# Kernel tuning notes

Measured on AMD Instinct MI355X. Metric: run time of the kernel, lower is better.

The kernel has to match this reference:

```python
import jax, jax.numpy as jnp
import numpy as np

SCALE = 8
NUM_CLASSES = 15
IGNORE_THRES = 0.5
# anchors for scale=8 divided by scale
GRID_ANCHOR = jnp.array([[96.0 / 8, 230.0 / 8], [79.0 / 8, 186.0 / 8], [81.0 / 8, 133.0 / 8]], dtype=jnp.float32)  # [3,2]


def _bce_sum(p, t, mask):
    # torch BCELoss(reduction='sum') with log clamped at -100, restricted to mask
    lp = jnp.maximum(jnp.log(p), -100.0)
    ln = jnp.maximum(jnp.log(1.0 - p), -100.0)
    return jnp.sum(-(t * lp + (1.0 - t) * ln) * mask)


def setup_inputs() -> dict:
    key = jax.random.key(0)
    k1, k2, k3 = jax.random.split(key, 3)
    nB, nG = 128, 52
    x = jax.random.normal(k1, (nB, 3 * (NUM_CLASSES + 5), nG, nG), dtype=jnp.float32)
    boxes = jax.random.uniform(k2, (nB, 4), minval=0.1, maxval=0.6)  # cx,cy,w,h in (0,1)
    cls = jax.random.randint(k3, (nB, 1), 0, NUM_CLASSES).astype(jnp.float32)
    labels = jnp.concatenate([boxes, cls], axis=-1)  # [nB,5]
    return {"x": x, "labels": labels}


def reference(x, labels):
    nB, nG = x.shape[0], x.shape[2]
    pred = x.reshape(nB, 3, NUM_CLASSES + 5, nG, nG).transpose(0, 1, 3, 4, 2)  # [B,3,G,G,20]
    px = jax.nn.sigmoid(pred[..., 0])
    py = jax.nn.sigmoid(pred[..., 1])
    pw = pred[..., 2]
    ph = pred[..., 3]
    conf = jax.nn.sigmoid(pred[..., 4])
    cls = jax.nn.softmax(pred[..., 5:], axis=-1)
    pred_boxs = jnp.stack([px, py, pw, ph], axis=-1)  # [B,3,G,G,4]
    out = jnp.concatenate([
        pred_boxs.reshape(nB, -1, 4) * SCALE,
        conf.reshape(nB, -1, 1),
        cls.reshape(nB, -1, NUM_CLASSES),
    ], axis=-1)

    # ---- build_targets (vectorized; one target per image as in original loop) ----
    tb = labels[:, :4] * nG  # boxes in grid units [B,4]
    gx, gy, gw, gh = tb[:, 0], tb[:, 1], tb[:, 2], tb[:, 3]
    gi = gx.astype(jnp.int32)
    gj = gy.astype(jnp.int32)
    gcls = labels[:, 4].astype(jnp.int32)

    # wh-IoU anchors vs targets -> [3,B]
    aw, ah = GRID_ANCHOR[:, 0:1], GRID_ANCHOR[:, 1:2]
    inter_wh = jnp.minimum(aw, gw[None, :]) * jnp.minimum(ah, gh[None, :])
    ious = inter_wh / (aw * ah + 1e-16 + gw[None, :] * gh[None, :] - inter_wh)
    best_idx = jnp.argmax(ious, axis=0)  # [B]

    bidx = jnp.arange(nB)
    shape4 = (nB, 3, nG, nG)
    obj = jnp.zeros(shape4, jnp.float32).at[bidx, best_idx, gj, gi].set(1.0)

    noobj = jnp.ones(shape4, jnp.float32)
    arep = jnp.tile(jnp.arange(3), nB)
    brep = jnp.repeat(bidx, 3)
    jrep = jnp.repeat(gj, 3)
    irep = jnp.repeat(gi, 3)
    ign = (jnp.reshape(ious.T, (-1,)) > IGNORE_THRES).astype(jnp.float32)
    noobj = noobj.at[brep, arep, jrep, irep].mul(1.0 - ign)
    noobj = noobj.at[bidx, best_idx, gj, gi].set(0.0)

    gif = gi.astype(jnp.float32)
    gjf = gj.astype(jnp.float32)
    tx = jnp.zeros(shape4, jnp.float32).at[bidx, best_idx, gj, gi].set(gx - gif)
    ty = jnp.zeros(shape4, jnp.float32).at[bidx, best_idx, gj, gi].set(gy - gjf)
    tw = jnp.zeros(shape4, jnp.float32).at[bidx, best_idx, gj, gi].set(jnp.log(gw / GRID_ANCHOR[best_idx, 0] + 1e-16))
    th = jnp.zeros(shape4, jnp.float32).at[bidx, best_idx, gj, gi].set(jnp.log(gh / GRID_ANCHOR[best_idx, 1] + 1e-16))
    tcls = jnp.zeros(shape4 + (NUM_CLASSES,), jnp.float32).at[bidx, best_idx, gj, gi, gcls].set(1.0)

    # cls_mask: does argmax of predicted class at target cell match gt class
    pred_cls_at = cls[bidx, best_idx, gj, gi]  # [B,15]
    cls_hit = (jnp.argmax(pred_cls_at, axis=-1) == gcls).astype(jnp.float32)
    cls_mask = jnp.zeros(shape4, jnp.float32).at[bidx, best_idx, gj, gi].set(cls_hit)

    # iou between pred box at target cell and target box (cxcywh, +1 corner convention)
    pb = pred_boxs[bidx, best_idx, gj, gi]  # [B,4]
    b1x1, b1y1 = pb[:, 0] - pb[:, 2] / 2, pb[:, 1] - pb[:, 3] / 2
    b1x2, b1y2 = pb[:, 0] + pb[:, 2] / 2, pb[:, 1] + pb[:, 3] / 2
    b2x1, b2y1 = gx - gw / 2, gy - gh / 2
    b2x2, b2y2 = gx + gw / 2, gy + gh / 2
    iw = jnp.clip(jnp.minimum(b1x2, b2x2) - jnp.maximum(b1x1, b2x1) + 1, 0)
    ih = jnp.clip(jnp.minimum(b1y2, b2y2) - jnp.maximum(b1y1, b2y1) + 1, 0)
    inter = iw * ih
    a1 = (b1x2 - b1x1 + 1) * (b1y2 - b1y1 + 1)
    a2 = (b2x2 - b2x1 + 1) * (b2y2 - b2y1 + 1)
    iou_vec = inter / (a1 + a2 - inter + 1e-16)
    iou_scores = jnp.zeros(shape4, jnp.float32).at[bidx, best_idx, gj, gi].set(iou_vec)

    tconf = obj
    # ---- losses (boolean-mask indexing replaced by masked sums) ----
    loss_x = jnp.sum(jnp.abs(px - tx) * obj)
    loss_y = jnp.sum(jnp.abs(py - ty) * obj)
    loss_w = jnp.sum(jnp.abs(pw - tw) * obj)
    loss_h = jnp.sum(jnp.abs(ph - th) * obj)
    loss_conf = _bce_sum(conf, tconf, obj) + 100.0 * _bce_sum(conf, tconf, noobj)
    loss_cls = _bce_sum(cls, tcls, obj[..., None])
    loss = loss_x + loss_y + loss_w + loss_h + loss_conf + loss_cls
    return (loss, out)
```

## Files before the change

### kernel.cpp

```cpp
#include <hip/hip_runtime.h>
#include <math.h>

#define NB    128
#define NG    52
#define NGG   2704
#define NA    3
#define NCLS  15
#define NCH   20
#define NQ    8112
#define TOTAL 1038336
#define BLK   256
#define NBLK  (TOTAL/BLK)
#define WPB   (BLK/64)
#define FPW   (64*NCH)
#define NPART (NBLK*WPB)

typedef float f4 __attribute__((ext_vector_type(4)));

__global__ __launch_bounds__(BLK) void main_kernel(const float* __restrict__ x,
                                                   const float* __restrict__ labels,
                                                   float* __restrict__ out,
                                                   float* __restrict__ partials) {
    __shared__ __align__(16) float sm[WPB][FPW];

    int t = threadIdx.x;
    int w = t >> 6;
    int l = t & 63;
    int cell = blockIdx.x * BLK + t;
    int b  = cell / NQ;
    int r  = cell - b * NQ;
    int a  = r / NGG;
    int ji = r - a * NGG;

    const float* __restrict__ xp = x + ((size_t)(b*60 + a*20)) * NGG + ji;
    float z[NCH];
    #pragma unroll
    for (int c = 0; c < NCH; c++) z[c] = xp[c * NGG];

    float v[NCH];
    float conf = 1.0f / (1.0f + __expf(-z[4]));
    v[0] = 8.0f / (1.0f + __expf(-z[0]));
    v[1] = 8.0f / (1.0f + __expf(-z[1]));
    v[2] = 8.0f * z[2];
    v[3] = 8.0f * z[3];
    v[4] = conf;
    float m = z[5];
    #pragma unroll
    for (int c = 6; c < NCH; c++) m = fmaxf(m, z[c]);
    float s = 0.0f;
    #pragma unroll
    for (int c = 0; c < NCLS; c++) { v[5+c] = __expf(z[5+c] - m); s += v[5+c]; }
    float inv = 1.0f / s;
    #pragma unroll
    for (int c = 0; c < NCLS; c++) v[5+c] *= inv;

    float gx = labels[b*5+0] * (float)NG;
    float gy = labels[b*5+1] * (float)NG;
    float gw = labels[b*5+2] * (float)NG;
    float gh = labels[b*5+3] * (float)NG;
    int  gcls = (int)labels[b*5+4];
    int gi = (int)gx, gj = (int)gy;
    float gwgh = gw * gh;
    float i0 = fminf(12.0f,   gw) * fminf(28.75f,  gh);
    float i1 = fminf(9.875f,  gw) * fminf(23.25f,  gh);
    float i2 = fminf(10.125f, gw) * fminf(16.625f, gh);
    float iou0 = i0 / (345.0f      + 1e-16f + gwgh - i0);
    float iou1 = i1 / (229.59375f  + 1e-16f + gwgh - i1);
    float iou2 = i2 / (168.328125f + 1e-16f + gwgh - i2);
    int best = 0; float bv = iou0;
    if (iou1 > bv) { best = 1; bv = iou1; }
    if (iou2 > bv) { best = 2; bv = iou2; }
    float ioua = (a == 0) ? iou0 : ((a == 1) ? iou1 : iou2);
    bool at_t   = (ji == gj * NG + gi);
    bool isbest = (a == best);

    float tsum = 0.0f;
    if (!(at_t && (isbest || ioua > 0.5f)))
        tsum = -100.0f * fmaxf(__logf(1.0f - conf), -100.0f);
    if (at_t && isbest) {
        tsum += -fmaxf(__logf(conf), -100.0f);
        float txv = gx - (float)gi;
        float tyv = gy - (float)gj;
        float abw = (best == 0) ? 12.0f  : ((best == 1) ? 9.875f : 10.125f);
        float abh = (best == 0) ? 28.75f : ((best == 1) ? 23.25f : 16.625f);
        float twv = __logf(gw / abw + 1e-16f);
        float thv = __logf(gh / abh + 1e-16f);
        tsum += fabsf(v[0]*0.125f - txv) + fabsf(v[1]*0.125f - tyv)
              + fabsf(v[2]*0.125f - twv) + fabsf(v[3]*0.125f - thv);
        #pragma unroll
        for (int c = 0; c < NCLS; c++) {
            float p = v[5+c];
            tsum += (c == gcls) ? -fmaxf(__logf(p),        -100.0f)
                                : -fmaxf(__logf(1.0f - p), -100.0f);
        }
    }

    float* __restrict__ smw = sm[w];
    int base = l * NCH - 3;
    #pragma unroll
    for (int c = 0; c < NCH; c++) {
        int L = base + c;
        if (L < 0) L += FPW;
        smw[L] = v[c];
    }

    #pragma unroll
    for (int off = 32; off > 0; off >>= 1) tsum += __shfl_down(tsum, off, 64);

    int cell0 = blockIdx.x * BLK + w * 64;
    size_t gf = 1 + (size_t)cell0 * NCH;
    f4* __restrict__ op = (f4*)(out + gf + 3);
    const f4* __restrict__ sp = (const f4*)smw;
    #pragma unroll
    for (int k = 0; k < 5; k++) {
        int q = k * 64 + l;
        if (q < (FPW - 4) / 4) __builtin_nontemporal_store(sp[q], &op[q]);
    }
    if (l == 0) {
        out[gf + 0]       = smw[FPW - 3];
        out[gf + 1]       = smw[FPW - 2];
        out[gf + 2]       = smw[FPW - 1];
        out[gf + FPW - 1] = smw[FPW - 4];
        partials[blockIdx.x * WPB + w] = tsum;
    }
}

__global__ __launch_bounds__(1024) void finish_kernel(const float* __restrict__ partials,
                                                      float* __restrict__ out) {
    int t = threadIdx.x;
    float s = 0.0f;
    #pragma unroll
    for (int k = 0; k < NPART/1024 + 1; k++) {
        int q = k * 1024 + t;
        if (q < NPART) s += partials[q];
    }
    __shared__ float red[1024];
    red[t] = s;
    __syncthreads();
    for (int k = 512; k > 0; k >>= 1) {
        if (t < k) red[t] += red[t + k];
        __syncthreads();
    }
    if (t == 0) out[0] = red[0];
}

extern "C" void kernel_launch(void* const* d_in, const int* in_sizes, int n_in,
                              void* d_out, int out_size, void* d_ws, size_t ws_size,
                              hipStream_t stream) {
    const float* x      = (const float*)d_in[0];
    const float* labels = (const float*)d_in[1];
    float* out = (float*)d_out;
    float* ws  = (float*)d_ws;

    hipLaunchKernelGGL(main_kernel,   dim3(NBLK), dim3(BLK),  0, stream, x, labels, out, ws);
    hipLaunchKernelGGL(finish_kernel, dim3(1),    dim3(1024), 0, stream, ws, out);
}
```

Before: 154.8 us.

## Process four cells per thread with vectorized loads and swizzled LDS staging

Each thread now handles four consecutive grid cells and loads its input channels as float4 vectors instead of scalar loads. Blocks shrink to 128 threads covering 512 cells, and the LDS staging buffer is enlarged and XOR-swizzled to limit bank conflicts when writing 20-float rows and reading them back as float4. This cuts load instruction count and amortizes label/IoU setup across cells, at the cost of higher register pressure and fewer total threads, which may reduce occupancy.

```diff
diff --git a/kernel.cpp b/kernel.cpp
--- a/kernel.cpp
+++ b/kernel.cpp
@@ -9,50 +9,39 @@
 #define NCH   20
 #define NQ    8112
 #define TOTAL 1038336
-#define BLK   256
-#define NBLK  (TOTAL/BLK)
-#define WPB   (BLK/64)
-#define FPW   (64*NCH)
-#define NPART (NBLK*WPB)
+#define BLK   128
+#define CPT   4
+#define WCELLS 256
+#define BCELLS 512
+#define NBLK  (TOTAL/BCELLS)
+#define FPW   (WCELLS*NCH)
+#define NQ4   ((FPW-4)/4)
+#define NPART (NBLK*2)
 
 typedef float f4 __attribute__((ext_vector_type(4)));
+
+__device__ __forceinline__ int swz(int L) { return L ^ (((L >> 7) & 7) << 2); }
 
 __global__ __launch_bounds__(BLK) void main_kernel(const float* __restrict__ x,
                                                    const float* __restrict__ labels,
                                                    float* __restrict__ out,
                                                    float* __restrict__ partials) {
-    __shared__ __align__(16) float sm[WPB][FPW];
+    __shared__ __align__(16) float sm[2][FPW];
 
     int t = threadIdx.x;
     int w = t >> 6;
     int l = t & 63;
-    int cell = blockIdx.x * BLK + t;
-    int b  = cell / NQ;
-    int r  = cell - b * NQ;
+    int cell0 = (blockIdx.x * BLK + t) * CPT;
+    int b  = cell0 / NQ;
+    int r  = cell0 - b * NQ;
     int a  = r / NGG;
-    int ji = r - a * NGG;
+    int ji0 = r - a * NGG;
 
-    const float* __restrict__ xp = x + ((size_t)(b*60 + a*20)) * NGG + ji;
-    float z[NCH];
+    const f4* __restrict__ xp4 =
+        (const f4*)(x + ((size_t)(b*60 + a*20)) * NGG) + (ji0 >> 2);
+    f4 z4[NCH];
     #pragma unroll
-    for (int c = 0; c < NCH; c++) z[c] = xp[c * NGG];
-
-    float v[NCH];
-    float conf = 1.0f / (1.0f + __expf(-z[4]));
-    v[0] = 8.0f / (1.0f + __expf(-z[0]));
-    v[1] = 8.0f / (1.0f + __expf(-z[1]));
-    v[2] = 8.0f * z[2];
-    v[3] = 8.0f * z[3];
-    v[4] = conf;
-    float m = z[5];
-    #pragma unroll
-    for (int c = 6; c < NCH; c++) m = fmaxf(m, z[c]);
-    float s = 0.0f;
-    #pragma unroll
-    for (int c = 0; c < NCLS; c++) { v[5+c] = __expf(z[5+c] - m); s += v[5+c]; }
-    float inv = 1.0f / s;
-    #pragma unroll
-    for (int c = 0; c < NCLS; c++) v[5+c] *= inv;
+    for (int c = 0; c < NCH; c++) z4[c] = xp4[c * (NGG/4)];
 
     float gx = labels[b*5+0] * (float)NG;
     float gy = labels[b*5+1] * (float)NG;
@@ -60,6 +49,7 @@
     float gh = labels[b*5+3] * (float)NG;
     int  gcls = (int)labels[b*5+4];
     int gi = (int)gx, gj = (int)gy;
+    int target = gj * NG + gi;
     float gwgh = gw * gh;
     float i0 = fminf(12.0f,   gw) * fminf(28.75f,  gh);
     float i1 = fminf(9.875f,  gw) * fminf(23.25f,  gh);
@@ -71,57 +61,85 @@
     if (iou1 > bv) { best = 1; bv = iou1; }
     if (iou2 > bv) { best = 2; bv = iou2; }
     float ioua = (a == 0) ? iou0 : ((a == 1) ? iou1 : iou2);
-    bool at_t   = (ji == gj * NG + gi);
     bool isbest = (a == best);
 
     float tsum = 0.0f;
-    if (!(at_t && (isbest || ioua > 0.5f)))
-        tsum = -100.0f * fmaxf(__logf(1.0f - conf), -100.0f);
-    if (at_t && isbest) {
-        tsum += -fmaxf(__logf(conf), -100.0f);
-        float txv = gx - (float)gi;
-        float tyv = gy - (float)gj;
-        float abw = (best == 0) ? 12.0f  : ((best == 1) ? 9.875f : 10.125f);
-        float abh = (best == 0) ? 28.75f : ((best == 1) ? 23.25f : 16.625f);
-        float twv = __logf(gw / abw + 1e-16f);
-        float thv = __logf(gh / abh + 1e-16f);
-        tsum += fabsf(v[0]*0.125f - txv) + fabsf(v[1]*0.125f - tyv)
-              + fabsf(v[2]*0.125f - twv) + fabsf(v[3]*0.125f - thv);
+    float* __restrict__ smw = sm[w];
+
+    #pragma unroll
+    for (int i = 0; i < CPT; i++) {
+        float z[NCH];
         #pragma unroll
-        for (int c = 0; c < NCLS; c++) {
-            float p = v[5+c];
-            tsum += (c == gcls) ? -fmaxf(__logf(p),        -100.0f)
-                                : -fmaxf(__logf(1.0f - p), -100.0f);
+        for (int c = 0; c < NCH; c++) z[c] = z4[c][i];
+
+        float v[NCH];
+        float conf = 1.0f / (1.0f + __expf(-z[4]));
+        v[0] = 8.0f / (1.0f + __expf(-z[0]));
+        v[1] = 8.0f / (1.0f + __expf(-z[1]));
+        v[2] = 8.0f * z[2];
+        v[3] = 8.0f * z[3];
+        v[4] = conf;
+        float m = z[5];
+        #pragma unroll
+        for (int c = 6; c < NCH; c++) m = fmaxf(m, z[c]);
+        float s = 0.0f;
+        #pragma unroll
+        for (int c = 0; c < NCLS; c++) { v[5+c] = __expf(z[5+c] - m); s += v[5+c]; }
+        float inv = 1.0f / s;
+        #pragma unroll
+        for (int c = 0; c < NCLS; c++) v[5+c] *= inv;
+
+        bool at_t = (ji0 + i == target);
+        if (!(at_t && (isbest || ioua > 0.5f)))
+            tsum += -100.0f * fmaxf(__logf(1.0f - conf), -100.0f);
+        if (at_t && isbest) {
+            tsum += -fmaxf(__logf(conf), -100.0f);
+            float txv = gx - (float)gi;
+            float tyv = gy - (float)gj;
+            float abw = (best == 0) ? 12.0f  : ((best == 1) ? 9.875f : 10.125f);
+            float abh = (best == 0) ? 28.75f : ((best == 1) ? 23.25f : 16.625f);
+            float twv = __logf(gw / abw + 1e-16f);
+            float thv = __logf(gh / abh + 1e-16f);
+            tsum += fabsf(v[0]*0.125f - txv) + fabsf(v[1]*0.125f - tyv)
+                  + fabsf(v[2]*0.125f - twv) + fabsf(v[3]*0.125f - thv);
+            #pragma unroll
+            for (int c = 0; c < NCLS; c++) {
+                float p = v[5+c];
+                tsum += (c == gcls) ? -fmaxf(__logf(p),        -100.0f)
+                                    : -fmaxf(__logf(1.0f - p), -100.0f);
+            }
         }
-    }
 
-    float* __restrict__ smw = sm[w];
-    int base = l * NCH - 3;
-    #pragma unroll
-    for (int c = 0; c < NCH; c++) {
-        int L = base + c;
-        if (L < 0) L += FPW;
-        smw[L] = v[c];
+        int base = (l * CPT + i) * NCH - 3;
+        #pragma unroll
+        for (int c = 0; c < NCH; c++) {
+            int L = base + c;
+            if (L < 0) L += FPW;
+            smw[swz(L)] = v[c];
+        }
     }
 
     #pragma unroll
     for (int off = 32; off > 0; off >>= 1) tsum += __shfl_down(tsum, off, 64);
 
-    int cell0 = blockIdx.x * BLK + w * 64;
-    size_t gf = 1 + (size_t)cell0 * NCH;
+    int wcell0 = blockIdx.x * BCELLS + w * WCELLS;
+    size_t gf = 1 + (size_t)wcell0 * NCH;
     f4* __restrict__ op = (f4*)(out + gf + 3);
     const f4* __restrict__ sp = (const f4*)smw;
     #pragma unroll
-    for (int k = 0; k < 5; k++) {
+    for (int k = 0; k < 20; k++) {
         int q = k * 64 + l;
-        if (q < (FPW - 4) / 4) __builtin_nontemporal_store(sp[q], &op[q]);
+        if (q < NQ4) {
+            f4 val = sp[q ^ ((q >> 5) & 7)];
+            __builtin_nontemporal_store(val, &op[q]);
+        }
     }
     if (l == 0) {
-        out[gf + 0]       = smw[FPW - 3];
-        out[gf + 1]       = smw[FPW - 2];
-        out[gf + 2]       = smw[FPW - 1];
-        out[gf + FPW - 1] = smw[FPW - 4];
-        partials[blockIdx.x * WPB + w] = tsum;
+        out[gf + 0]       = smw[swz(FPW - 3)];
+        out[gf + 1]       = smw[swz(FPW - 2)];
+        out[gf + 2]       = smw[swz(FPW - 1)];
+        out[gf + FPW - 1] = smw[swz(FPW - 4)];
+        partials[blockIdx.x * 2 + w] = tsum;
     }
 }
 
```

Result: no change. 157.4 us (+1.7%).
